# Performance work log

Hardware: AMD Instinct MI355X
Metric: run time of the kernel (lower is better)

## Reference

```python
import jax, jax.numpy as jnp
import numpy as np

# T=timepoints, B=batch, N=neurons, H=lstm hidden, D=INPUT_DIM, P=len(PEOPLE)
T, B, N, H, D, P = 512, 64, 256, 64, 128, 64


def setup_inputs() -> dict:
    key = jax.random.key(0)
    ks = jax.random.split(key, 11)
    s = lambda k, shape, sc: jax.random.normal(k, shape, dtype=jnp.float32) * sc
    return {
        "input": s(ks[0], (T, B, D), 1.0),
        "W2n": s(ks[1], (N, D), D ** -0.5),      # linear2neurons weight [N, D]
        "b2n": s(ks[2], (N,), D ** -0.5),
        "W_ih": s(ks[3], (4 * H, 1), 1.0),        # LSTMCell input weights (input_size=1)
        "W_hh": s(ks[4], (4 * H, H), H ** -0.5),  # LSTMCell recurrent weights
        "b_ih": s(ks[5], (4 * H,), H ** -0.5),
        "b_hh": s(ks[6], (4 * H,), H ** -0.5),
        "Wg": s(ks[7], (1, H), H ** -0.5),        # linearLSTM: H -> 1 gain
        "bg": s(ks[8], (1,), H ** -0.5),
        "Wout": s(ks[9], (P, N), N ** -0.5),      # neurons2output
        "bout": s(ks[10], (P,), N ** -0.5),
    }


def reference(input, W2n, b2n, W_ih, W_hh, b_ih, b_hh, Wg, bg, Wout, bout):
    # Drive to every neuron for all timesteps: [T, B, N]
    x2n = jnp.einsum('tbd,nd->tbn', input, W2n) + b2n
    h0 = jnp.zeros((B, N, H), input.dtype)
    g0 = jnp.zeros((B, N), input.dtype)
    bias = b_ih + b_hh
    w_ih = W_ih[:, 0]  # [4H], since lstm input is scalar per neuron
    wg = Wg[0]         # [H]

    def step(carry, inp):
        h, c, g_prev1, g_prev2 = carry  # g_prev1 = g_{t-1}, g_prev2 = g_{t-2}
        xt, t = inp                     # xt: [B, N]
        # PyTorch LSTMCell gate order: i, f, g, o
        gates = xt[..., None] * w_ih + jnp.einsum('bnh,gh->bng', h, W_hh) + bias  # [B,N,4H]
        i_g, f_g, c_g, o_g = jnp.split(gates, 4, axis=-1)
        c = jax.nn.sigmoid(f_g) * c + jax.nn.sigmoid(i_g) * jnp.tanh(c_g)
        h = jax.nn.sigmoid(o_g) * jnp.tanh(c)
        g_t = jnp.einsum('bnh,h->bn', h, wg) + bg[0]  # gain at time t, [B,N]
        # original list semantics: t=0 uses g_t itself, t=1 uses constant 1, t>=2 uses g_{t-2}
        gain = jnp.where(t == 0, g_t, jnp.where(t == 1, jnp.ones_like(g_t), g_prev2))
        out = gain * jax.nn.softplus(xt - 1.0)  # log(1 + exp(x - 1))
        return (h, c, g_t, g_prev1), out

    _, out_neurons = jax.lax.scan(step, (h0, h0, g0, g0), (x2n, jnp.arange(T)))
    # out_neurons: [T, B, N] -> final projection to people logits [T, B, P]
    return jnp.einsum('tbn,pn->tbp', out_neurons, Wout) + bout
```

## Files before the change

kernel.cpp:

```cpp
#include <hip/hip_runtime.h>
#include <hip/hip_bf16.h>


typedef __attribute__((ext_vector_type(4))) float f32x4;
typedef __attribute__((ext_vector_type(4))) short s16x4;
typedef __attribute__((ext_vector_type(8))) short s16x8;

__device__ inline short bf16r(float f) {
    unsigned u = __builtin_bit_cast(unsigned, f);
    u += 0x7fffu + ((u >> 16) & 1u);
    return (short)(u >> 16);
}
__device__ inline float bf2f(short s) {
    unsigned u = ((unsigned)(unsigned short)s) << 16;
    return __builtin_bit_cast(float, u);
}
__device__ inline float sigf(float x) {
    return __builtin_amdgcn_rcpf(1.f + __builtin_amdgcn_exp2f(x * -1.4426950408889634f));
}
__device__ inline float tanh_fast(float x) {
    return 1.f - 2.f * __builtin_amdgcn_rcpf(1.f + __builtin_amdgcn_exp2f(x * 2.885390081777927f));
}

#if __has_builtin(__builtin_amdgcn_mfma_f32_16x16x16bf16_1k)
#define HAVE_MFMA16 1
__device__ inline f32x4 mfma16(s16x4 a, s16x4 b, f32x4 c) {
    return __builtin_amdgcn_mfma_f32_16x16x16bf16_1k(a, b, c, 0, 0, 0);
}
#else
#define HAVE_MFMA16 0
__device__ inline s16x8 cat8(s16x4 a, s16x4 b) {
    s16x8 r;
    r[0]=a[0]; r[1]=a[1]; r[2]=a[2]; r[3]=a[3];
    r[4]=b[0]; r[5]=b[1]; r[6]=b[2]; r[7]=b[3];
    return r;
}
#endif

__global__ __launch_bounds__(256) void gemm_xwT(
    const float* __restrict__ X, const float* __restrict__ Wt,
    const float* __restrict__ bias, float* __restrict__ Out,
    int N, int K)
{
    __shared__ float Xs[32][68];
    __shared__ float Ws[32][68];
    const int tid = threadIdx.x;
    const int tx = tid & 15, ty = tid >> 4;
    const int m0 = blockIdx.x * 64, n0 = blockIdx.y * 64;
    const int kq = tid & 7, mr = tid >> 3;

    float acc[4][4];
#pragma unroll
    for (int i = 0; i < 4; ++i)
#pragma unroll
        for (int j = 0; j < 4; ++j) acc[i][j] = 0.f;

    for (int kc = 0; kc < K; kc += 32) {
#pragma unroll
        for (int rr = 0; rr < 2; ++rr) {
            const int m = mr + rr * 32;
            f32x4 xv = *(const f32x4*)(X + (size_t)(m0 + m) * K + kc + kq * 4);
            f32x4 wv = *(const f32x4*)(Wt + (size_t)(n0 + m) * K + kc + kq * 4);
#pragma unroll
            for (int j = 0; j < 4; ++j) { Xs[kq*4 + j][m] = xv[j]; Ws[kq*4 + j][m] = wv[j]; }
        }
        __syncthreads();
#pragma unroll
        for (int k = 0; k < 32; ++k) {
            f32x4 a = *(const f32x4*)&Xs[k][ty * 4];
            f32x4 b = *(const f32x4*)&Ws[k][tx * 4];
#pragma unroll
            for (int i = 0; i < 4; ++i)
#pragma unroll
                for (int j = 0; j < 4; ++j)
                    acc[i][j] = __builtin_fmaf(a[i], b[j], acc[i][j]);
        }
        __syncthreads();
    }
    f32x4 bv = *(const f32x4*)(bias + n0 + tx * 4);
#pragma unroll
    for (int i = 0; i < 4; ++i) {
        f32x4 o;
#pragma unroll
        for (int j = 0; j < 4; ++j) o[j] = acc[i][j] + bv[j];
        *(f32x4*)(Out + (size_t)(m0 + ty * 4 + i) * N + n0 + tx * 4) = o;
    }
}

__global__ __launch_bounds__(64, 1) void lstm_scan(
    const float* __restrict__ x2n,
    const float* __restrict__ W_hh,
    const float* __restrict__ w_ih,
    const float* __restrict__ b_ih,
    const float* __restrict__ b_hh,
    const float* __restrict__ wg,
    const float* __restrict__ bg,
    float* __restrict__ ON)
{
    const int lane = threadIdx.x & 63;
    const int c15 = lane & 15, g4 = lane >> 4;
    const int cellbase = blockIdx.x * 16;

    s16x4 afw[4][16];
#pragma unroll
    for (int nt = 0; nt < 16; ++nt) {
        const float* wrow = W_hh + (size_t)(nt * 16 + c15) * 64;
#pragma unroll
        for (int ks = 0; ks < 4; ++ks) {
            f32x4 w = *(const f32x4*)(wrow + ks * 16 + g4 * 4);
            s16x4 bb;
#pragma unroll
            for (int e = 0; e < 4; ++e) bb[e] = bf16r(w[e]);
            afw[ks][nt] = bb;
        }
    }

    s16x4 afx[16];
#pragma unroll
    for (int nt = 0; nt < 16; ++nt) {
        const int g = nt * 16 + c15;
        const float wi = w_ih[g];
        const float bs = b_ih[g] + b_hh[g];
        const short wh = bf16r(wi);
        const short wl = bf16r(wi - bf2f(wh));
        const short bh_ = bf16r(bs);
        const short bl_ = bf16r(bs - bf2f(bh_));
        s16x4 v = (s16x4){0, 0, 0, 0};
        if (g4 == 0) { v[0] = wh; v[1] = wh; v[2] = wl; v[3] = bh_; }
        else if (g4 == 1) { v[0] = bl_; }
        afx[nt] = v;
    }

    f32x4 wg_l[4];
#pragma unroll
    for (int q = 0; q < 4; ++q) wg_l[q] = *(const f32x4*)(wg + q * 16 + g4 * 4);
    const float bg0 = bg[0];
    const short one_bf = (short)0x3F80;

    f32x4 cst[4];
    s16x4 bh[4];
#pragma unroll
    for (int q = 0; q < 4; ++q) {
        cst[q] = (f32x4){0.f, 0.f, 0.f, 0.f};
        bh[q] = (s16x4){0, 0, 0, 0};
    }
    float gp1 = 0.f, gp2 = 0.f;

    float xs = x2n[cellbase + c15];

    for (int t = 0; t < 512; ++t) {
        const short xh = bf16r(xs);
        const short xl = bf16r(xs - bf2f(xh));
        s16x4 bx = (s16x4){0, 0, 0, 0};
        if (g4 == 0) { bx[0] = xh; bx[1] = xl; bx[2] = xh; bx[3] = one_bf; }
        else if (g4 == 1) { bx[0] = one_bf; }
        const float xs_cur = xs;
        if (t < 511) xs = x2n[(size_t)(t + 1) * 16384 + cellbase + c15];

        f32x4 acc[16];
        const f32x4 zero4 = (f32x4){0.f, 0.f, 0.f, 0.f};
#if HAVE_MFMA16
#pragma unroll
        for (int nt = 0; nt < 16; ++nt) acc[nt] = mfma16(afx[nt], bx, zero4);
#pragma unroll
        for (int ks = 0; ks < 4; ++ks)
#pragma unroll
            for (int nt = 0; nt < 16; ++nt)
                acc[nt] = mfma16(afw[ks][nt], bh[ks], acc[nt]);
#else
        {
            const s16x4 z4 = (s16x4){0, 0, 0, 0};
            s16x8 bx8 = cat8(bx, z4);
            s16x8 b01 = cat8(bh[0], bh[1]);
            s16x8 b23 = cat8(bh[2], bh[3]);
#pragma unroll
            for (int nt = 0; nt < 16; ++nt) {
                acc[nt] = __builtin_amdgcn_mfma_f32_16x16x32_bf16(cat8(afx[nt], z4), bx8, zero4, 0, 0, 0);
                acc[nt] = __builtin_amdgcn_mfma_f32_16x16x32_bf16(cat8(afw[0][nt], afw[1][nt]), b01, acc[nt], 0, 0, 0);
                acc[nt] = __builtin_amdgcn_mfma_f32_16x16x32_bf16(cat8(afw[2][nt], afw[3][nt]), b23, acc[nt], 0, 0, 0);
            }
        }
#endif

        f32x4 hvf[4];
#pragma unroll
        for (int q = 0; q < 4; ++q) {
            f32x4 cn, hn;
#pragma unroll
            for (int e = 0; e < 4; ++e) {
                const float iv = acc[q][e], fv = acc[q + 4][e];
                const float gv = acc[q + 8][e], ov = acc[q + 12][e];
                const float c2 = sigf(fv) * cst[q][e] + sigf(iv) * tanh_fast(gv);
                cn[e] = c2;
                hn[e] = sigf(ov) * tanh_fast(c2);
            }
            cst[q] = cn;
            hvf[q] = hn;
        }

#pragma unroll
        for (int q = 0; q < 4; ++q) {
            s16x4 b;
#pragma unroll
            for (int e = 0; e < 4; ++e) b[e] = bf16r(hvf[q][e]);
            bh[q] = b;
        }

        float gpart = 0.f;
#pragma unroll
        for (int q = 0; q < 4; ++q)
#pragma unroll
            for (int e = 0; e < 4; ++e)
                gpart = __builtin_fmaf(hvf[q][e], wg_l[q][e], gpart);
        gpart += __shfl_xor(gpart, 16, 64);
        gpart += __shfl_xor(gpart, 32, 64);
        const float gcur = gpart + bg0;

        const float gain = (t == 0) ? gcur : ((t == 1) ? 1.f : gp2);
        const float x1 = xs_cur - 1.f;
        const float sp = fmaxf(x1, 0.f) +
            0.6931471805599453f * __builtin_amdgcn_logf(
                1.f + __builtin_amdgcn_exp2f(-1.4426950408889634f * fabsf(x1)));
        if (g4 == 0) ON[(size_t)t * 16384 + cellbase + c15] = gain * sp;

        gp2 = gp1;
        gp1 = gcur;
    }
}

extern "C" void kernel_launch(void* const* d_in, const int* in_sizes, int n_in,
                              void* d_out, int out_size, void* d_ws, size_t ws_size,
                              hipStream_t stream)
{
    const float* input = (const float*)d_in[0];
    const float* W2n   = (const float*)d_in[1];
    const float* b2n   = (const float*)d_in[2];
    const float* W_ih  = (const float*)d_in[3];
    const float* W_hh  = (const float*)d_in[4];
    const float* b_ih  = (const float*)d_in[5];
    const float* b_hh  = (const float*)d_in[6];
    const float* Wg    = (const float*)d_in[7];
    const float* bg    = (const float*)d_in[8];
    const float* Wout  = (const float*)d_in[9];
    const float* bout  = (const float*)d_in[10];

    float* x2n = (float*)d_ws;
    float* ON  = x2n + (size_t)512 * 16384;

    gemm_xwT<<<dim3(512, 4), 256, 0, stream>>>(input, W2n, b2n, x2n, 256, 128);

    lstm_scan<<<1024, 64, 0, stream>>>(x2n, W_hh, W_ih, b_ih, b_hh, Wg, bg, ON);

    gemm_xwT<<<dim3(512, 1), 256, 0, stream>>>(ON, Wout, bout, (float*)d_out, 64, 256);
}
```

Measured before the change: 885.1 us.

## Split each LSTM cell group across two waves exchanging hidden state via LDS

Each block now runs two wavefronts, each owning half of the hidden units (two of four q-slices across all four gates). The waves exchange their bf16 hidden halves each step through a double-buffered LDS array, and the gain partials are combined through a small shared ring buffer. This halves the MFMA and activation work per wave on the serial recurrence critical path. In exchange it adds a block barrier and LDS traffic every timestep, and the gain bookkeeping is restructured, including a deferred t=0 write.

New measurement: 1.841 ms. 108% more time.

```diff
diff --git a/kernel.cpp b/kernel.cpp
--- a/kernel.cpp
+++ b/kernel.cpp
@@ -87,7 +87,7 @@
     }
 }
 
-__global__ __launch_bounds__(64, 1) void lstm_scan(
+__global__ __launch_bounds__(128, 2) void lstm_scan(
     const float* __restrict__ x2n,
     const float* __restrict__ W_hh,
     const float* __restrict__ w_ih,
@@ -97,27 +97,36 @@
     const float* __restrict__ bg,
     float* __restrict__ ON)
 {
-    const int lane = threadIdx.x & 63;
+    __shared__ short hbuf[2][4][64][4];
+    __shared__ float gbuf[4][16];
+
+    const int tid = threadIdx.x;
+    const int w = tid >> 6;
+    const int lane = tid & 63;
     const int c15 = lane & 15, g4 = lane >> 4;
     const int cellbase = blockIdx.x * 16;
-
-    s16x4 afw[4][16];
-#pragma unroll
-    for (int nt = 0; nt < 16; ++nt) {
+    const int q0 = 2 * w;
+    const int ko = 2 - q0;
+
+    s16x4 afw[4][8];
+#pragma unroll
+    for (int lt = 0; lt < 8; ++lt) {
+        const int nt = (lt >> 1) * 4 + q0 + (lt & 1);
         const float* wrow = W_hh + (size_t)(nt * 16 + c15) * 64;
 #pragma unroll
         for (int ks = 0; ks < 4; ++ks) {
-            f32x4 w = *(const f32x4*)(wrow + ks * 16 + g4 * 4);
+            f32x4 wv = *(const f32x4*)(wrow + ks * 16 + g4 * 4);
             s16x4 bb;
 #pragma unroll
-            for (int e = 0; e < 4; ++e) bb[e] = bf16r(w[e]);
-            afw[ks][nt] = bb;
-        }
-    }
-
-    s16x4 afx[16];
-#pragma unroll
-    for (int nt = 0; nt < 16; ++nt) {
+            for (int e = 0; e < 4; ++e) bb[e] = bf16r(wv[e]);
+            afw[ks][lt] = bb;
+        }
+    }
+
+    s16x4 afx[8];
+#pragma unroll
+    for (int lt = 0; lt < 8; ++lt) {
+        const int nt = (lt >> 1) * 4 + q0 + (lt & 1);
         const int g = nt * 16 + c15;
         const float wi = w_ih[g];
         const float bs = b_ih[g] + b_hh[g];
@@ -128,45 +137,56 @@
         s16x4 v = (s16x4){0, 0, 0, 0};
         if (g4 == 0) { v[0] = wh; v[1] = wh; v[2] = wl; v[3] = bh_; }
         else if (g4 == 1) { v[0] = bl_; }
-        afx[nt] = v;
-    }
-
-    f32x4 wg_l[4];
-#pragma unroll
-    for (int q = 0; q < 4; ++q) wg_l[q] = *(const f32x4*)(wg + q * 16 + g4 * 4);
+        afx[lt] = v;
+    }
+
+    f32x4 wg_l[2];
+#pragma unroll
+    for (int ql = 0; ql < 2; ++ql)
+        wg_l[ql] = *(const f32x4*)(wg + (q0 + ql) * 16 + g4 * 4);
     const float bg0 = bg[0];
     const short one_bf = (short)0x3F80;
 
-    f32x4 cst[4];
-    s16x4 bh[4];
-#pragma unroll
-    for (int q = 0; q < 4; ++q) {
-        cst[q] = (f32x4){0.f, 0.f, 0.f, 0.f};
-        bh[q] = (s16x4){0, 0, 0, 0};
-    }
-    float gp1 = 0.f, gp2 = 0.f;
+    f32x4 cst[2];
+    s16x4 bown[2];
+#pragma unroll
+    for (int ql = 0; ql < 2; ++ql) {
+        cst[ql] = (f32x4){0.f, 0.f, 0.f, 0.f};
+        bown[ql] = (s16x4){0, 0, 0, 0};
+        *(s16x4*)&hbuf[0][q0 + ql][lane][0] = (s16x4){0, 0, 0, 0};
+    }
+    __syncthreads();
 
     float xs = x2n[cellbase + c15];
+    float gp1 = 0.f, gp2 = 0.f, sp0 = 0.f;
 
     for (int t = 0; t < 512; ++t) {
-        const short xh = bf16r(xs);
-        const short xl = bf16r(xs - bf2f(xh));
+        const int p = t & 1;
+
+        s16x4 bh[4];
+        bh[ko]     = *(const s16x4*)&hbuf[p][ko][lane][0];
+        bh[ko + 1] = *(const s16x4*)&hbuf[p][ko + 1][lane][0];
+        bh[q0]     = bown[0];
+        bh[q0 + 1] = bown[1];
+
+        const float xs_cur = xs;
+        const short xh = bf16r(xs_cur);
+        const short xl = bf16r(xs_cur - bf2f(xh));
         s16x4 bx = (s16x4){0, 0, 0, 0};
         if (g4 == 0) { bx[0] = xh; bx[1] = xl; bx[2] = xh; bx[3] = one_bf; }
         else if (g4 == 1) { bx[0] = one_bf; }
-        const float xs_cur = xs;
         if (t < 511) xs = x2n[(size_t)(t + 1) * 16384 + cellbase + c15];
 
-        f32x4 acc[16];
+        f32x4 acc[8];
         const f32x4 zero4 = (f32x4){0.f, 0.f, 0.f, 0.f};
 #if HAVE_MFMA16
 #pragma unroll
-        for (int nt = 0; nt < 16; ++nt) acc[nt] = mfma16(afx[nt], bx, zero4);
+        for (int lt = 0; lt < 8; ++lt) acc[lt] = mfma16(afx[lt], bx, zero4);
 #pragma unroll
         for (int ks = 0; ks < 4; ++ks)
 #pragma unroll
-            for (int nt = 0; nt < 16; ++nt)
-                acc[nt] = mfma16(afw[ks][nt], bh[ks], acc[nt]);
+            for (int lt = 0; lt < 8; ++lt)
+                acc[lt] = mfma16(afw[ks][lt], bh[ks], acc[lt]);
 #else
         {
             const s16x4 z4 = (s16x4){0, 0, 0, 0};
@@ -174,57 +194,71 @@
             s16x8 b01 = cat8(bh[0], bh[1]);
             s16x8 b23 = cat8(bh[2], bh[3]);
 #pragma unroll
-            for (int nt = 0; nt < 16; ++nt) {
-                acc[nt] = __builtin_amdgcn_mfma_f32_16x16x32_bf16(cat8(afx[nt], z4), bx8, zero4, 0, 0, 0);
-                acc[nt] = __builtin_amdgcn_mfma_f32_16x16x32_bf16(cat8(afw[0][nt], afw[1][nt]), b01, acc[nt], 0, 0, 0);
-                acc[nt] = __builtin_amdgcn_mfma_f32_16x16x32_bf16(cat8(afw[2][nt], afw[3][nt]), b23, acc[nt], 0, 0, 0);
+            for (int lt = 0; lt < 8; ++lt) {
+                acc[lt] = __builtin_amdgcn_mfma_f32_16x16x32_bf16(cat8(afx[lt], z4), bx8, zero4, 0, 0, 0);
+                acc[lt] = __builtin_amdgcn_mfma_f32_16x16x32_bf16(cat8(afw[0][lt], afw[1][lt]), b01, acc[lt], 0, 0, 0);
+                acc[lt] = __builtin_amdgcn_mfma_f32_16x16x32_bf16(cat8(afw[2][lt], afw[3][lt]), b23, acc[lt], 0, 0, 0);
             }
         }
 #endif
 
-        f32x4 hvf[4];
-#pragma unroll
-        for (int q = 0; q < 4; ++q) {
+        f32x4 hvf[2];
+#pragma unroll
+        for (int ql = 0; ql < 2; ++ql) {
             f32x4 cn, hn;
 #pragma unroll
             for (int e = 0; e < 4; ++e) {
-                const float iv = acc[q][e], fv = acc[q + 4][e];
-                const float gv = acc[q + 8][e], ov = acc[q + 12][e];
-                const float c2 = sigf(fv) * cst[q][e] + sigf(iv) * tanh_fast(gv);
+                const float iv = acc[ql][e], fv = acc[2 + ql][e];
+                const float gv = acc[4 + ql][e], ov = acc[6 + ql][e];
+                const float c2 = sigf(fv) * cst[ql][e] + sigf(iv) * tanh_fast(gv);
                 cn[e] = c2;
                 hn[e] = sigf(ov) * tanh_fast(c2);
             }
-            cst[q] = cn;
-            hvf[q] = hn;
-        }
-
-#pragma unroll
-        for (int q = 0; q < 4; ++q) {
+            cst[ql] = cn;
+            hvf[ql] = hn;
+        }
+
+#pragma unroll
+        for (int ql = 0; ql < 2; ++ql) {
             s16x4 b;
 #pragma unroll
-            for (int e = 0; e < 4; ++e) b[e] = bf16r(hvf[q][e]);
-            bh[q] = b;
+            for (int e = 0; e < 4; ++e) b[e] = bf16r(hvf[ql][e]);
+            bown[ql] = b;
+            *(s16x4*)&hbuf[p ^ 1][q0 + ql][lane][0] = b;
         }
 
         float gpart = 0.f;
 #pragma unroll
-        for (int q = 0; q < 4; ++q)
+        for (int ql = 0; ql < 2; ++ql)
 #pragma unroll
             for (int e = 0; e < 4; ++e)
-                gpart = __builtin_fmaf(hvf[q][e], wg_l[q][e], gpart);
+                gpart = __builtin_fmaf(hvf[ql][e], wg_l[ql][e], gpart);
         gpart += __shfl_xor(gpart, 16, 64);
         gpart += __shfl_xor(gpart, 32, 64);
-        const float gcur = gpart + bg0;
-
-        const float gain = (t == 0) ? gcur : ((t == 1) ? 1.f : gp2);
-        const float x1 = xs_cur - 1.f;
-        const float sp = fmaxf(x1, 0.f) +
-            0.6931471805599453f * __builtin_amdgcn_logf(
-                1.f + __builtin_amdgcn_exp2f(-1.4426950408889634f * fabsf(x1)));
-        if (g4 == 0) ON[(size_t)t * 16384 + cellbase + c15] = gain * sp;
-
-        gp2 = gp1;
-        gp1 = gcur;
+
+        if (w == 1) {
+            if (g4 == 0) gbuf[t & 3][c15] = gpart;
+        } else {
+            const float x1 = xs_cur - 1.f;
+            const float sp = fmaxf(x1, 0.f) +
+                0.6931471805599453f * __builtin_amdgcn_logf(
+                    1.f + __builtin_amdgcn_exp2f(-1.4426950408889634f * fabsf(x1)));
+            if (t == 0) {
+                sp0 = sp;
+            } else if (t == 1) {
+                if (g4 == 0) ON[(size_t)16384 + cellbase + c15] = sp;
+            } else {
+                const float gain = gp2 + gbuf[(t - 2) & 3][c15] + bg0;
+                if (g4 == 0) {
+                    ON[(size_t)t * 16384 + cellbase + c15] = gain * sp;
+                    if (t == 2) ON[cellbase + c15] = gain * sp0;
+                }
+            }
+            gp2 = gp1;
+            gp1 = gpart;
+        }
+
+        __syncthreads();
     }
 }
 
@@ -249,7 +283,7 @@
 
     gemm_xwT<<<dim3(512, 4), 256, 0, stream>>>(input, W2n, b2n, x2n, 256, 128);
 
-    lstm_scan<<<1024, 64, 0, stream>>>(x2n, W_hh, W_ih, b_ih, b_hh, Wg, bg, ON);
+    lstm_scan<<<1024, 128, 0, stream>>>(x2n, W_hh, W_ih, b_ih, b_hh, Wg, bg, ON);
 
     gemm_xwT<<<dim3(512, 1), 256, 0, stream>>>(ON, Wout, bout, (float*)d_out, 64, 256);
 }
```

## Fold exp2 scaling into LSTM weights, share reciprocals, defer gain reduction

Applied to the files above, without the earlier changes.

Pre-scales the recurrent weights, input weights and biases by -log2(e), or 2·log2(e) for the cell gate, so the MFMA outputs feed exp2 directly with no per-step multiply. Sigmoid/tanh products are then rewritten so one reciprocal covers two values: paired forget gates share one, and each input·tanh and output·tanh product uses a single one. The h to bf16 conversion uses the hardware v_cvt_pk_bf16_f32 pack. The gain shuffle reduction is moved to the start of the step two iterations later, with special handling for t=0..2, which takes the cross-lane shuffles off the recurrent critical path. Risks include precision changes from scaling before bf16 rounding, and extra clamps needed to avoid exp2 overflow.

New measurement: 950.0 us. 7.3% more time.

```diff
diff --git a/kernel.cpp b/kernel.cpp
--- a/kernel.cpp
+++ b/kernel.cpp
@@ -5,6 +5,7 @@
 typedef __attribute__((ext_vector_type(4))) float f32x4;
 typedef __attribute__((ext_vector_type(4))) short s16x4;
 typedef __attribute__((ext_vector_type(8))) short s16x8;
+typedef __attribute__((ext_vector_type(2))) unsigned u32x2;
 
 __device__ inline short bf16r(float f) {
     unsigned u = __builtin_bit_cast(unsigned, f);
@@ -15,11 +16,10 @@
     unsigned u = ((unsigned)(unsigned short)s) << 16;
     return __builtin_bit_cast(float, u);
 }
-__device__ inline float sigf(float x) {
-    return __builtin_amdgcn_rcpf(1.f + __builtin_amdgcn_exp2f(x * -1.4426950408889634f));
-}
-__device__ inline float tanh_fast(float x) {
-    return 1.f - 2.f * __builtin_amdgcn_rcpf(1.f + __builtin_amdgcn_exp2f(x * 2.885390081777927f));
+__device__ inline unsigned pkbf(float a, float b) {
+    unsigned r;
+    asm("v_cvt_pk_bf16_f32 %0, %1, %2" : "=v"(r) : "v"(a), "v"(b));
+    return r;
 }
 
 #if __has_builtin(__builtin_amdgcn_mfma_f32_16x16x16bf16_1k)
@@ -29,13 +29,13 @@
 }
 #else
 #define HAVE_MFMA16 0
+#endif
 __device__ inline s16x8 cat8(s16x4 a, s16x4 b) {
     s16x8 r;
     r[0]=a[0]; r[1]=a[1]; r[2]=a[2]; r[3]=a[3];
     r[4]=b[0]; r[5]=b[1]; r[6]=b[2]; r[7]=b[3];
     return r;
 }
-#endif
 
 __global__ __launch_bounds__(256) void gemm_xwT(
     const float* __restrict__ X, const float* __restrict__ Wt,
@@ -101,26 +101,26 @@
     const int c15 = lane & 15, g4 = lane >> 4;
     const int cellbase = blockIdx.x * 16;
 
+    const float L2E = 1.4426950408889634f;
+
     s16x4 afw[4][16];
+    s16x4 afx[16];
 #pragma unroll
     for (int nt = 0; nt < 16; ++nt) {
+        const int type = nt >> 2;
+        const float sc = (type == 2) ? (2.f * L2E) : (-L2E);
         const float* wrow = W_hh + (size_t)(nt * 16 + c15) * 64;
 #pragma unroll
         for (int ks = 0; ks < 4; ++ks) {
             f32x4 w = *(const f32x4*)(wrow + ks * 16 + g4 * 4);
             s16x4 bb;
 #pragma unroll
-            for (int e = 0; e < 4; ++e) bb[e] = bf16r(w[e]);
+            for (int e = 0; e < 4; ++e) bb[e] = bf16r(w[e] * sc);
             afw[ks][nt] = bb;
         }
-    }
-
-    s16x4 afx[16];
-#pragma unroll
-    for (int nt = 0; nt < 16; ++nt) {
         const int g = nt * 16 + c15;
-        const float wi = w_ih[g];
-        const float bs = b_ih[g] + b_hh[g];
+        const float wi = w_ih[g] * sc;
+        const float bs = (b_ih[g] + b_hh[g]) * sc;
         const short wh = bf16r(wi);
         const short wl = bf16r(wi - bf2f(wh));
         const short bh_ = bf16r(bs);
@@ -144,18 +144,22 @@
         cst[q] = (f32x4){0.f, 0.f, 0.f, 0.f};
         bh[q] = (s16x4){0, 0, 0, 0};
     }
-    float gp1 = 0.f, gp2 = 0.f;
+    float gpraw1 = 0.f, gpraw2 = 0.f, sp0 = 0.f;
 
     float xs = x2n[cellbase + c15];
 
     for (int t = 0; t < 512; ++t) {
-        const short xh = bf16r(xs);
-        const short xl = bf16r(xs - bf2f(xh));
+        float g2r = gpraw2;
+        g2r += __shfl_xor(g2r, 16, 64);
+        g2r += __shfl_xor(g2r, 32, 64);
+
+        const float xs_cur = xs;
+        const short xh = bf16r(xs_cur);
+        const short xl = bf16r(xs_cur - bf2f(xh));
         s16x4 bx = (s16x4){0, 0, 0, 0};
         if (g4 == 0) { bx[0] = xh; bx[1] = xl; bx[2] = xh; bx[3] = one_bf; }
         else if (g4 == 1) { bx[0] = one_bf; }
-        const float xs_cur = xs;
-        if (t < 511) xs = x2n[(size_t)(t + 1) * 16384 + cellbase + c15];
+        xs = x2n[(size_t)((t + 1) & 511) * 16384 + cellbase + c15];
 
         f32x4 acc[16];
         const f32x4 zero4 = (f32x4){0.f, 0.f, 0.f, 0.f};
@@ -184,27 +188,45 @@
 
         f32x4 hvf[4];
 #pragma unroll
-        for (int q = 0; q < 4; ++q) {
-            f32x4 cn, hn;
+        for (int qp = 0; qp < 2; ++qp) {
+            const int qa = 2 * qp, qb = qa + 1;
+            f32x4 cna, cnb, hna, hnb;
 #pragma unroll
             for (int e = 0; e < 4; ++e) {
-                const float iv = acc[q][e], fv = acc[q + 4][e];
-                const float gv = acc[q + 8][e], ov = acc[q + 12][e];
-                const float c2 = sigf(fv) * cst[q][e] + sigf(iv) * tanh_fast(gv);
-                cn[e] = c2;
-                hn[e] = sigf(ov) * tanh_fast(c2);
+                const float ufa = __builtin_amdgcn_exp2f(fminf(acc[qa + 4][e], 43.f));
+                const float ufb = __builtin_amdgcn_exp2f(fminf(acc[qb + 4][e], 43.f));
+                const float dfa = 1.f + ufa, dfb = 1.f + ufb;
+                const float rf = __builtin_amdgcn_rcpf(dfa * dfb);
+                const float sfa = rf * dfb, sfb = rf * dfa;
+
+                const float uia = __builtin_amdgcn_exp2f(acc[qa][e]);
+                const float uib = __builtin_amdgcn_exp2f(acc[qb][e]);
+                const float vga = __builtin_amdgcn_exp2f(fminf(acc[qa + 8][e], 43.f));
+                const float vgb = __builtin_amdgcn_exp2f(fminf(acc[qb + 8][e], 43.f));
+                const float pa = (vga - 1.f) *
+                    __builtin_amdgcn_rcpf((1.f + uia) * (1.f + vga));
+                const float pb = (vgb - 1.f) *
+                    __builtin_amdgcn_rcpf((1.f + uib) * (1.f + vgb));
+
+                const float ca = __builtin_fmaf(sfa, cst[qa][e], pa);
+                const float cb = __builtin_fmaf(sfb, cst[qb][e], pb);
+                cna[e] = ca; cnb[e] = cb;
+
+                const float uoa = __builtin_amdgcn_exp2f(acc[qa + 12][e]);
+                const float uob = __builtin_amdgcn_exp2f(acc[qb + 12][e]);
+                const float vca = __builtin_amdgcn_exp2f(fminf(2.8853900817779268f * ca, 43.f));
+                const float vcb = __builtin_amdgcn_exp2f(fminf(2.8853900817779268f * cb, 43.f));
+                hna[e] = (vca - 1.f) * __builtin_amdgcn_rcpf((1.f + uoa) * (1.f + vca));
+                hnb[e] = (vcb - 1.f) * __builtin_amdgcn_rcpf((1.f + uob) * (1.f + vcb));
             }
-            cst[q] = cn;
-            hvf[q] = hn;
-        }
-
-#pragma unroll
-        for (int q = 0; q < 4; ++q) {
-            s16x4 b;
-#pragma unroll
-            for (int e = 0; e < 4; ++e) b[e] = bf16r(hvf[q][e]);
-            bh[q] = b;
-        }
+            cst[qa] = cna; cst[qb] = cnb;
+            hvf[qa] = hna; hvf[qb] = hnb;
+        }
+
+#pragma unroll
+        for (int q = 0; q < 4; ++q)
+            bh[q] = __builtin_bit_cast(s16x4,
+                        (u32x2){pkbf(hvf[q][0], hvf[q][1]), pkbf(hvf[q][2], hvf[q][3])});
 
         float gpart = 0.f;
 #pragma unroll
@@ -212,19 +234,24 @@
 #pragma unroll
             for (int e = 0; e < 4; ++e)
                 gpart = __builtin_fmaf(hvf[q][e], wg_l[q][e], gpart);
-        gpart += __shfl_xor(gpart, 16, 64);
-        gpart += __shfl_xor(gpart, 32, 64);
-        const float gcur = gpart + bg0;
-
-        const float gain = (t == 0) ? gcur : ((t == 1) ? 1.f : gp2);
+
         const float x1 = xs_cur - 1.f;
         const float sp = fmaxf(x1, 0.f) +
             0.6931471805599453f * __builtin_amdgcn_logf(
                 1.f + __builtin_amdgcn_exp2f(-1.4426950408889634f * fabsf(x1)));
-        if (g4 == 0) ON[(size_t)t * 16384 + cellbase + c15] = gain * sp;
-
-        gp2 = gp1;
-        gp1 = gcur;
+        if (t >= 2) {
+            const float gain = g2r + bg0;
+            if (g4 == 0) {
+                ON[(size_t)t * 16384 + cellbase + c15] = gain * sp;
+                if (t == 2) ON[cellbase + c15] = gain * sp0;
+            }
+        } else if (t == 1) {
+            if (g4 == 0) ON[(size_t)16384 + cellbase + c15] = sp;
+        } else {
+            sp0 = sp;
+        }
+        gpraw2 = gpraw1;
+        gpraw1 = gpart;
     }
 }
 
```
